# Kernel tuning notes

Measured on AMD Instinct MI355X. Metric: run time of the kernel, lower is better.

Reference implementation:

```python
import jax, jax.numpy as jnp
import numpy as np

N_NODES = 50000
N_EDGES = 600000
IN_CH = 128
HID = 256
OUT_FEAT = 256
OUT_CH = 128
EPS = 1e-12


def _sage_conv(x, src, dst, mask_f, Wl, bl, Wr, n_nodes):
    # PyG SAGEConv: out = lin_l(mean_{j in N(i)} x_j) + lin_r(x_i); L2-normalize rows.
    msg = x[src] * mask_f[:, None]                                  # [E, d] gather
    agg = jax.ops.segment_sum(msg, dst, num_segments=n_nodes)      # [N, d]
    cnt = jax.ops.segment_sum(mask_f, dst, num_segments=n_nodes)   # [N]
    agg = agg / jnp.maximum(cnt, 1.0)[:, None]                      # mean over kept edges
    out = agg @ Wl.T + bl + x @ Wr.T                                 # [N, h]
    nrm = jnp.maximum(jnp.linalg.norm(out, axis=-1, keepdims=True), EPS)
    return out / nrm


def setup_inputs() -> dict:
    key = jax.random.key(0)
    ks = jax.random.split(key, 12)
    x = jax.random.normal(ks[0], (N_NODES, IN_CH), dtype=jnp.float32)
    edge_index = jax.random.randint(ks[1], (2, N_EDGES), 0, N_NODES, dtype=jnp.int32)
    edge_mask = jax.random.bernoulli(ks[2], 0.7, (N_EDGES,))  # dropout_edge p=0.3 keep mask

    def lin(k, fan_out, fan_in):
        s = 1.0 / np.sqrt(fan_in)
        return jax.random.uniform(k, (fan_out, fan_in), jnp.float32, -s, s)

    W1l = lin(ks[3], HID, IN_CH)
    b1 = jnp.zeros((HID,), jnp.float32)
    W1r = lin(ks[4], HID, IN_CH)
    Ws = lin(ks[5], HID, IN_CH)
    bs = jnp.zeros((HID,), jnp.float32)
    W2l = lin(ks[6], OUT_FEAT, HID)
    b2 = jnp.zeros((OUT_FEAT,), jnp.float32)
    W2r = lin(ks[7], OUT_FEAT, HID)
    Wo = lin(ks[8], OUT_CH, OUT_FEAT)
    bo = jnp.zeros((OUT_CH,), jnp.float32)
    return {"x": x, "edge_index": edge_index, "edge_mask": edge_mask,
            "W1l": W1l, "b1": b1, "W1r": W1r, "Ws": Ws, "bs": bs,
            "W2l": W2l, "b2": b2, "W2r": W2r, "Wo": Wo, "bo": bo}


def reference(x, edge_index, edge_mask, W1l, b1, W1r, Ws, bs, W2l, b2, W2r, Wo, bo):
    src, dst = edge_index[0], edge_index[1]
    ones = jnp.ones((src.shape[0],), x.dtype)
    # conv1 uses all edges
    h = _sage_conv(x, src, dst, ones, W1l, b1, W1r, N_NODES)
    h = h + (x @ Ws.T + bs)
    h = jnp.tanh(h)
    # conv2 uses edge-dropped graph (mask = kept edges)
    mask_f = edge_mask.astype(x.dtype)
    h = jnp.tanh(_sage_conv(h, src, dst, mask_f, W2l, b2, W2r, N_NODES))
    return h @ Wo.T + bo
```

## Files before the change

### kernel.cpp

```cpp
#include <hip/hip_runtime.h>
#include <hip/hip_bf16.h>

#define N_NODES 50000
#define N_PAD   50048
#define N_EDGES 600000
#define IN_CH 128
#define HID 256
#define OUT_CH 128

typedef unsigned short u16;
typedef unsigned char u8;
typedef unsigned int u32;

typedef __attribute__((ext_vector_type(8))) short short8;
typedef __attribute__((ext_vector_type(4))) float f32x4;

typedef __attribute__((address_space(3))) u32 as3_u32;
typedef __attribute__((address_space(1))) const u32 as1_u32;

__device__ __forceinline__ float bf2f(u16 v) {
    unsigned u = ((unsigned)v) << 16;
    return __uint_as_float(u);
}
__device__ __forceinline__ u16 f2bf(float f) {
    unsigned u = __float_as_uint(f);
    u += 0x7FFF + ((u >> 16) & 1);
    return (u16)(u >> 16);
}

__device__ __forceinline__ void async16(const void* g, void* l) {
    __builtin_amdgcn_global_load_lds((as1_u32*)g, (as3_u32*)l, 16, 0, 0);
}

__global__ void detect_kernel(const u16* __restrict__ xu, const u8* __restrict__ mb,
                              int* __restrict__ flags) {
    int lane = threadIdx.x & 63;

    int inr = 0;
    {
        u32 w0 = ((const u32*)xu)[lane * 2 + 0];
        u32 w1 = ((const u32*)xu)[lane * 2 + 1];
        u16 h[4] = {(u16)w0, (u16)(w0 >> 16), (u16)w1, (u16)(w1 >> 16)};
#pragma unroll
        for (int j = 0; j < 4; j++) {
            int e = (h[j] >> 7) & 0xFF;
            if (e >= 100 && e <= 133) inr++;
        }
    }

    int c1 = 0, c23 = 0, h3f_1 = 0, h3f_3 = 0;
#pragma unroll
    for (int t = 0; t < 16; t++) {
        u32 w = ((const u32*)mb)[t * 64 + lane];
        u8 b1 = (u8)(w >> 8), b2 = (u8)(w >> 16), b3 = (u8)(w >> 24);
        if (b1) c1++;
        if (b1 == 0x3F) h3f_1 = 1;
        if (b2) c23++;
        if (b3) c23++;
        if (b3 == 0x3F) h3f_3 = 1;
    }

#pragma unroll
    for (int off = 32; off > 0; off >>= 1) {
        inr   += __shfl_xor(inr, off, 64);
        c1    += __shfl_xor(c1, off, 64);
        c23   += __shfl_xor(c23, off, 64);
        h3f_1 |= __shfl_xor(h3f_1, off, 64);
        h3f_3 |= __shfl_xor(h3f_3, off, 64);
    }

    if (lane == 0 && blockIdx.x == 0) {
        flags[0] = (inr >= 200) ? 1 : 0;
        int fmt;
        if (h3f_1) fmt = 3;
        else if (h3f_3) fmt = 2;
        else if (c1 + c23 > 0) fmt = 0;
        else fmt = 1;
        flags[1] = fmt;
    }
}

#define NX (N_NODES * IN_CH)
__global__ void convert_all_kernel(const void* __restrict__ x,
                                   const void* __restrict__ W1l, const void* __restrict__ W1r,
                                   const void* __restrict__ Ws,
                                   const void* __restrict__ W2l, const void* __restrict__ W2r,
                                   const void* __restrict__ Wo,
                                   const void* __restrict__ b1, const void* __restrict__ bs,
                                   const void* __restrict__ b2, const void* __restrict__ bo,
                                   u16* __restrict__ xb, u16* __restrict__ Wc1,
                                   u16* __restrict__ Wsb, u16* __restrict__ Wc2,
                                   u16* __restrict__ Wob, float* __restrict__ biasf,
                                   const int* __restrict__ flags) {
    int i = blockIdx.x * blockDim.x + threadIdx.x;
    int isbf = flags[0];
    auto cv = [&](const void* s, int idx) -> u16 {
        return isbf ? ((const u16*)s)[idx] : f2bf(((const float*)s)[idx]);
    };
    if (i < NX) { xb[i] = cv(x, i); return; }
    i -= NX;
    if (i < 256 * 256) {
        int n = i >> 8, k = i & 255;
        const void* s = (k < 128) ? W1l : W1r;
        Wc1[i] = cv(s, n * 128 + (k & 127));
        return;
    }
    i -= 256 * 256;
    if (i < 256 * 128) { Wsb[i] = cv(Ws, i); return; }
    i -= 256 * 128;
    if (i < 256 * 512) {
        int n = i >> 9, k = i & 511;
        const void* s = (k < 256) ? W2l : W2r;
        Wc2[i] = cv(s, n * 256 + (k & 255));
        return;
    }
    i -= 256 * 512;
    if (i < 128 * 256) { Wob[i] = cv(Wo, i); return; }
    i -= 128 * 256;
    if (i < 896) {
        const void* s; int idx;
        if (i < 256)      { s = b1; idx = i; }
        else if (i < 512) { s = bs; idx = i - 256; }
        else if (i < 768) { s = b2; idx = i - 512; }
        else              { s = bo; idx = i - 768; }
        biasf[i] = isbf ? bf2f(((const u16*)s)[idx]) : ((const float*)s)[idx];
    }
}
#define CONV_TOTAL (NX + 256 * 256 + 256 * 128 + 256 * 512 + 128 * 256 + 896)

__global__ void hist_kernel(const int* __restrict__ ei, const void* __restrict__ em,
                            u32* __restrict__ degp, u32* __restrict__ rankp,
                            const int* __restrict__ flags) {
    int i = blockIdx.x * blockDim.x + threadIdx.x;
    if (i >= N_EDGES) return;
    int d = ei[N_EDGES + i];
    int fmt = flags[1];
    bool keep;
    if (fmt == 0)      keep = ((const u8*)em)[i] != 0;
    else if (fmt == 1) keep = ((const int*)em)[i] != 0;
    else if (fmt == 2) keep = ((const float*)em)[i] != 0.f;
    else               keep = ((const u16*)em)[i] != 0;
    u32 inc = keep ? 0x10001u : 1u;
    u32 old = atomicAdd(&degp[d], inc);
    rankp[i] = (old & 0xffffu) | (keep ? (old & 0xffff0000u) : 0xffff0000u);
}

__global__ void partial_kernel(const u32* __restrict__ degp, u32* __restrict__ partial) {
    __shared__ u32 sh[256];
    int t = threadIdx.x;
    int i = blockIdx.x * 256 + t;
    sh[t] = (i < N_NODES) ? degp[i] : 0;
    __syncthreads();
    for (int s = 128; s > 0; s >>= 1) {
        if (t < s) sh[t] += sh[t + s];
        __syncthreads();
    }
    if (t == 0) partial[blockIdx.x] = sh[0];
}

__global__ void scanp_kernel(const u32* __restrict__ partial, int* __restrict__ pscan, int nb) {
    __shared__ int sh[256];
    int t = threadIdx.x;
    u32 pv = (t < nb) ? partial[t] : 0;
    int v1 = pv & 0xffff, v2 = pv >> 16;
    sh[t] = v1;
    __syncthreads();
    for (int o = 1; o < 256; o <<= 1) {
        int u = (t >= o) ? sh[t - o] : 0;
        __syncthreads();
        sh[t] += u;
        __syncthreads();
    }
    if (t < nb) pscan[t] = sh[t] - v1;
    __syncthreads();
    sh[t] = v2;
    __syncthreads();
    for (int o = 1; o < 256; o <<= 1) {
        int u = (t >= o) ? sh[t - o] : 0;
        __syncthreads();
        sh[t] += u;
        __syncthreads();
    }
    if (t < nb) pscan[nb + t] = sh[t] - v2;
}

__global__ void rowptr_kernel(const u32* __restrict__ degp, const int* __restrict__ pscan,
                              int* __restrict__ row_ptr, int* __restrict__ row_ptr2, int nb) {
    __shared__ u32 sh[256];
    int t = threadIdx.x;
    int i = blockIdx.x * 256 + t;
    u32 v = (i < N_NODES) ? degp[i] : 0;
    sh[t] = v;
    __syncthreads();
    for (int o = 1; o < 256; o <<= 1) {
        u32 u = (t >= o) ? sh[t - o] : 0;
        __syncthreads();
        sh[t] += u;
        __syncthreads();
    }
    u32 ex = sh[t] - v;
    if (i <= N_NODES) {
        row_ptr[i]  = pscan[blockIdx.x] + (int)(ex & 0xffff);
        row_ptr2[i] = pscan[nb + blockIdx.x] + (int)(ex >> 16);
    }
}

__global__ void scatter_csr_kernel(const int* __restrict__ ei, const u32* __restrict__ rankp,
                                   const int* __restrict__ row_ptr, const int* __restrict__ row_ptr2,
                                   int* __restrict__ srcs, int* __restrict__ srcs2) {
    int i = blockIdx.x * blockDim.x + threadIdx.x;
    if (i >= N_EDGES) return;
    int d = ei[N_EDGES + i];
    int s = ei[i];
    u32 rp = rankp[i];
    srcs[row_ptr[d] + (int)(rp & 0xffffu)] = s;
    u32 kr = rp >> 16;
    if (kr != 0xffffu) srcs2[row_ptr2[d] + (int)kr] = s;
}

__global__ __launch_bounds__(256) void gather1_kernel(const int* __restrict__ row_ptr,
                                                      const int* __restrict__ srcs,
                                                      const u16* __restrict__ xb,
                                                      u16* __restrict__ aggb) {
    int wid = (blockIdx.x * blockDim.x + threadIdx.x) >> 6;
    int lane = threadIdx.x & 63;
    if (wid >= N_NODES) return;
    int start = row_ptr[wid], end = row_ptr[wid + 1];
    int dg = end - start;
    int sv = (lane < dg) ? srcs[start + lane] : 0;
    float a0 = 0.f, a1 = 0.f, b0 = 0.f, b1 = 0.f;
    float c0 = 0.f, c1 = 0.f, d0 = 0.f, d1 = 0.f;
    int n = dg < 64 ? dg : 64;
    int e = 0;
    for (; e + 4 <= n; e += 4) {
        int s0 = __builtin_amdgcn_readlane(sv, e);
        int s1 = __builtin_amdgcn_readlane(sv, e + 1);
        int s2 = __builtin_amdgcn_readlane(sv, e + 2);
        int s3 = __builtin_amdgcn_readlane(sv, e + 3);
        u32 v0 = *(const u32*)(xb + (size_t)s0 * IN_CH + lane * 2);
        u32 v1 = *(const u32*)(xb + (size_t)s1 * IN_CH + lane * 2);
        u32 v2 = *(const u32*)(xb + (size_t)s2 * IN_CH + lane * 2);
        u32 v3 = *(const u32*)(xb + (size_t)s3 * IN_CH + lane * 2);
        a0 += bf2f((u16)v0); a1 += bf2f((u16)(v0 >> 16));
        b0 += bf2f((u16)v1); b1 += bf2f((u16)(v1 >> 16));
        c0 += bf2f((u16)v2); c1 += bf2f((u16)(v2 >> 16));
        d0 += bf2f((u16)v3); d1 += bf2f((u16)(v3 >> 16));
    }
    for (; e < n; e++) {
        int s0 = __builtin_amdgcn_readlane(sv, e);
        u32 v0 = *(const u32*)(xb + (size_t)s0 * IN_CH + lane * 2);
        a0 += bf2f((u16)v0); a1 += bf2f((u16)(v0 >> 16));
    }
    for (e = 64; e < dg; e++) {
        int s0 = srcs[start + e];
        u32 v0 = *(const u32*)(xb + (size_t)s0 * IN_CH + lane * 2);
        a0 += bf2f((u16)v0); a1 += bf2f((u16)(v0 >> 16));
    }
    float inv = 1.f / fmaxf((float)dg, 1.f);
    float rx = (a0 + b0) + (c0 + d0);
    float ry = (a1 + b1) + (c1 + d1);
    u32 o = (u32)f2bf(rx * inv) | ((u32)f2bf(ry * inv) << 16);
    *(u32*)(aggb + (size_t)wid * IN_CH + lane * 2) = o;
}

__global__ __launch_bounds__(256) void gather2_kernel(const int* __restrict__ row_ptr2,
                                                      const int* __restrict__ srcs2,
                                                      const u16* __restrict__ h1b,
                                                      u16* __restrict__ aggb) {
    int wid = (blockIdx.x * blockDim.x + threadIdx.x) >> 6;
    int lane = threadIdx.x & 63;
    if (wid >= N_NODES) return;
    int start = row_ptr2[wid], end = row_ptr2[wid + 1];
    int dg = end - start;
    int sv = (lane < dg) ? srcs2[start + lane] : 0;
    float a0 = 0.f, a1 = 0.f, a2 = 0.f, a3 = 0.f;
    float b0 = 0.f, b1 = 0.f, b2 = 0.f, b3 = 0.f;
    float c0 = 0.f, c1 = 0.f, c2 = 0.f, c3 = 0.f;
    float d0 = 0.f, d1 = 0.f, d2 = 0.f, d3 = 0.f;
    int n = dg < 64 ? dg : 64;
    int e = 0;
    for (; e + 4 <= n; e += 4) {
        int s0 = __builtin_amdgcn_readlane(sv, e);
        int s1 = __builtin_amdgcn_readlane(sv, e + 1);
        int s2 = __builtin_amdgcn_readlane(sv, e + 2);
        int s3 = __builtin_amdgcn_readlane(sv, e + 3);
        uint2 v = *(const uint2*)(h1b + (size_t)s0 * HID + lane * 4);
        uint2 w = *(const uint2*)(h1b + (size_t)s1 * HID + lane * 4);
        uint2 y = *(const uint2*)(h1b + (size_t)s2 * HID + lane * 4);
        uint2 zz = *(const uint2*)(h1b + (size_t)s3 * HID + lane * 4);
        a0 += bf2f((u16)v.x); a1 += bf2f((u16)(v.x >> 16));
        a2 += bf2f((u16)v.y); a3 += bf2f((u16)(v.y >> 16));
        b0 += bf2f((u16)w.x); b1 += bf2f((u16)(w.x >> 16));
        b2 += bf2f((u16)w.y); b3 += bf2f((u16)(w.y >> 16));
        c0 += bf2f((u16)y.x); c1 += bf2f((u16)(y.x >> 16));
        c2 += bf2f((u16)y.y); c3 += bf2f((u16)(y.y >> 16));
        d0 += bf2f((u16)zz.x); d1 += bf2f((u16)(zz.x >> 16));
        d2 += bf2f((u16)zz.y); d3 += bf2f((u16)(zz.y >> 16));
    }
    for (; e < n; e++) {
        int s0 = __builtin_amdgcn_readlane(sv, e);
        uint2 v = *(const uint2*)(h1b + (size_t)s0 * HID + lane * 4);
        a0 += bf2f((u16)v.x); a1 += bf2f((u16)(v.x >> 16));
        a2 += bf2f((u16)v.y); a3 += bf2f((u16)(v.y >> 16));
    }
    for (e = 64; e < dg; e++) {
        int s0 = srcs2[start + e];
        uint2 v = *(const uint2*)(h1b + (size_t)s0 * HID + lane * 4);
        a0 += bf2f((u16)v.x); a1 += bf2f((u16)(v.x >> 16));
        a2 += bf2f((u16)v.y); a3 += bf2f((u16)(v.y >> 16));
    }
    float inv = 1.f / fmaxf((float)dg, 1.f);
    float r0 = (a0 + b0) + (c0 + d0);
    float r1 = (a1 + b1) + (c1 + d1);
    float r2 = (a2 + b2) + (c2 + d2);
    float r3 = (a3 + b3) + (c3 + d3);
    u32 o0 = (u32)f2bf(r0 * inv) | ((u32)f2bf(r1 * inv) << 16);
    u32 o1 = (u32)f2bf(r2 * inv) | ((u32)f2bf(r3 * inv) << 16);
    u16* p = aggb + (size_t)wid * HID + lane * 4;
    *(u32*)p = o0;
    *(u32*)(p + 2) = o1;
}

template<int MODE>
__global__ __launch_bounds__(256, 2) void gemm_staged(
    const u16* __restrict__ A0, const u16* __restrict__ A1,
    const u16* __restrict__ W0, const u16* __restrict__ W1,
    const float* __restrict__ bias0, const float* __restrict__ bias1,
    u16* __restrict__ outb, void* __restrict__ outv, const int* __restrict__ flags) {

    constexpr int NT  = (MODE == 3) ? 2 : 4;
    constexpr int Nw  = NT * 16;
    constexpr int NKS = (MODE == 1) ? 6 : ((MODE == 2) ? 8 : 4);
    constexpr int BBYTES = NT * 64 * 128;
    __shared__ __align__(16) u8 ldsmem[16384 + 2 * BBYTES];

    int tid = threadIdx.x;
    int w = tid >> 6, lane = tid & 63;
    int q = lane >> 4, c = lane & 15;
    int m_base = blockIdx.x * 64;
    int rj = lane >> 3, jj = lane & 7;
    int j16 = ((jj ^ rj) << 4);

    f32x4 acc[4][NT], acc2[4][NT];
    const f32x4 z = {0.f, 0.f, 0.f, 0.f};
#pragma unroll
    for (int mt = 0; mt < 4; mt++)
#pragma unroll
        for (int nt = 0; nt < NT; nt++) { acc[mt][nt] = z; acc2[mt][nt] = z; }

    auto stage = [&](int ks, int b) {
        const u16* ap; int astr, kta;
        const u16* wp; int wstr, ktw;
        if (MODE == 1) {
            astr = 128;
            if (ks < 2)      { ap = A0; kta = ks; }
            else if (ks < 4) { ap = A1; kta = ks - 2; }
            else             { ap = A1; kta = ks - 4; }
            if (ks < 4) { wp = W0; wstr = 256; ktw = ks; }
            else        { wp = W1; wstr = 128; ktw = ks - 4; }
        } else if (MODE == 2) {
            astr = 256;
            if (ks < 4) { ap = A0; kta = ks; } else { ap = A1; kta = ks - 4; }
            wp = W0; wstr = 512; ktw = ks;
        } else {
            astr = 256; ap = A0; kta = ks;
            wp = W0; wstr = 256; ktw = ks;
        }
#pragma unroll
        for (int t = 0; t < 2; t++) {
            int r = w * 16 + t * 8;
            const u8* g = (const u8*)(ap + (size_t)(m_base + r + rj) * astr) + kta * 128 + j16;
            async16(g, ldsmem + b * 8192 + r * 128);
        }
#pragma unroll
        for (int t = 0; t < NT * 2; t++) {
            int n = w * Nw + t * 8;
            const u8* g = (const u8*)(wp + (size_t)(n + rj) * wstr) + ktw * 128 + j16;
            async16(g, ldsmem + 16384 + b * BBYTES + n * 128);
        }
    };

    auto compute = [&](int b, f32x4 (*tgt)[NT]) {
        const u8* ab = ldsmem + b * 8192;
        const u8* bb = ldsmem + 16384 + b * BBYTES;
#pragma unroll
        for (int kk = 0; kk < 2; kk++) {
            int sA = (((kk * 4 + q) ^ (c & 7)) << 4);
            short8 af[4], bfr[NT];
#pragma unroll
            for (int mt = 0; mt < 4; mt++)
                af[mt] = *(const short8*)(ab + (mt * 16 + c) * 128 + sA);
#pragma unroll
            for (int nt = 0; nt < NT; nt++)
                bfr[nt] = *(const short8*)(bb + (w * Nw + nt * 16 + c) * 128 + sA);
#pragma unroll
            for (int mt = 0; mt < 4; mt++)
#pragma unroll
                for (int nt = 0; nt < NT; nt++)
                    tgt[mt][nt] = __builtin_amdgcn_mfma_f32_16x16x32_bf16(af[mt], bfr[nt], tgt[mt][nt], 0, 0, 0);
        }
    };

    stage(0, 0);
    int b = 0;
#pragma unroll
    for (int ks = 0; ks < NKS; ks++) {
        __syncthreads();
        if (ks + 1 < NKS) stage(ks + 1, b ^ 1);
        if (MODE == 1 && ks >= 4) compute(b, acc2);
        else                      compute(b, acc);
        b ^= 1;
    }
    __syncthreads();

    if (MODE == 3) {
        float bcol[NT];
#pragma unroll
        for (int nt = 0; nt < NT; nt++) bcol[nt] = bias0[w * Nw + nt * 16 + c];
        int isbf = flags[0];
#pragma unroll
        for (int mt = 0; mt < 4; mt++)
#pragma unroll
            for (int r = 0; r < 4; r++) {
                int row = m_base + mt * 16 + q * 4 + r;
                if (row < N_NODES) {
#pragma unroll
                    for (int nt = 0; nt < NT; nt++) {
                        float v = acc[mt][nt][r] + bcol[nt];
                        int col = w * Nw + nt * 16 + c;
                        if (isbf) ((u16*)outv)[(size_t)row * OUT_CH + col] = f2bf(v);
                        else      ((float*)outv)[(size_t)row * OUT_CH + col] = v;
                    }
                }
            }
    } else {
        float* redf = (float*)ldsmem;
        float bcol[NT], b2col[NT];
#pragma unroll
        for (int nt = 0; nt < NT; nt++) {
            int col = w * Nw + nt * 16 + c;
            bcol[nt] = bias0[col];
            if (MODE == 1) b2col[nt] = bias1[col];
        }
        float s[4][4];
#pragma unroll
        for (int mt = 0; mt < 4; mt++)
#pragma unroll
            for (int r = 0; r < 4; r++) {
                float t = 0.f;
#pragma unroll
                for (int nt = 0; nt < NT; nt++) {
                    float v = acc[mt][nt][r] + bcol[nt];
                    acc[mt][nt][r] = v;
                    t += v * v;
                }
                s[mt][r] = t;
            }
#pragma unroll
        for (int off = 1; off < 16; off <<= 1) {
#pragma unroll
            for (int mt = 0; mt < 4; mt++)
#pragma unroll
                for (int r = 0; r < 4; r++)
                    s[mt][r] += __shfl_xor(s[mt][r], off, 64);
        }
        if (c == 0) {
#pragma unroll
            for (int mt = 0; mt < 4; mt++)
#pragma unroll
                for (int r = 0; r < 4; r++)
                    redf[(mt * 16 + q * 4 + r) * 4 + w] = s[mt][r];
        }
        __syncthreads();
        if (tid < 64) {
            float t = redf[tid * 4] + redf[tid * 4 + 1] + redf[tid * 4 + 2] + redf[tid * 4 + 3];
            redf[256 + tid] = 1.f / fmaxf(sqrtf(t), 1e-12f);
        }
        __syncthreads();
#pragma unroll
        for (int mt = 0; mt < 4; mt++)
#pragma unroll
            for (int r = 0; r < 4; r++) {
                int rl = mt * 16 + q * 4 + r;
                int row = m_base + rl;
                if (row < N_NODES) {
                    float iv = redf[256 + rl];
#pragma unroll
                    for (int nt = 0; nt < NT; nt++) {
                        int col = w * Nw + nt * 16 + c;
                        float h;
                        if (MODE == 1) h = acc[mt][nt][r] * iv + acc2[mt][nt][r] + b2col[nt];
                        else           h = acc[mt][nt][r] * iv;
                        outb[(size_t)row * HID + col] = f2bf(tanhf(h));
                    }
                }
            }
    }
}

extern "C" void kernel_launch(void* const* d_in, const int* in_sizes, int n_in,
                              void* d_out, int out_size, void* d_ws, size_t ws_size,
                              hipStream_t stream) {
    const void* x    = d_in[0];
    const int*  ei   = (const int*)d_in[1];
    const void* em   = d_in[2];
    const void* W1l  = d_in[3];
    const void* b1   = d_in[4];
    const void* W1r  = d_in[5];
    const void* Ws   = d_in[6];
    const void* bs   = d_in[7];
    const void* W2l  = d_in[8];
    const void* b2   = d_in[9];
    const void* W2r  = d_in[10];
    const void* Wo   = d_in[11];
    const void* bo   = d_in[12];

    char* p = (char*)d_ws;
    auto carve = [&](size_t bytes) { char* r = p; p += (bytes + 63) & ~(size_t)63; return r; };
    int*   flags   = (int*)carve(256);
    u16*   xb      = (u16*)carve((size_t)N_PAD * IN_CH * 2);
    u16*   h1b     = (u16*)carve((size_t)N_PAD * HID * 2);
    u16*   aggb    = (u16*)carve((size_t)N_PAD * HID * 2);
    u16*   h2b     = (u16*)carve((size_t)N_PAD * HID * 2);
    u16*   Wc1     = (u16*)carve(256 * 256 * 2);
    u16*   Wsb     = (u16*)carve(256 * 128 * 2);
    u16*   Wc2     = (u16*)carve(256 * 512 * 2);
    u16*   Wob     = (u16*)carve(128 * 256 * 2);
    float* biasf   = (float*)carve(896 * 4);
    u32*   degp    = (u32*)carve(50176 * 4);
    int*   row_ptr = (int*)carve(50056 * 4);
    int*   row_ptr2= (int*)carve(50056 * 4);
    u32*   partial = (u32*)carve(256 * 4);
    int*   pscan   = (int*)carve(512 * 4);
    u32*   rankp   = (u32*)carve((size_t)N_EDGES * 4);
    int*   srcs    = (int*)carve((size_t)N_EDGES * 4);
    int*   srcs2   = (int*)carve((size_t)N_EDGES * 4);
    float* b1f = biasf, *bsf = biasf + 256, *b2f = biasf + 512, *bof = biasf + 768;
    (void)ws_size; (void)in_sizes; (void)n_in; (void)out_size;

    detect_kernel<<<1, 64, 0, stream>>>((const u16*)x, (const u8*)em, flags);

    convert_all_kernel<<<(CONV_TOTAL + 255) / 256, 256, 0, stream>>>(
        x, W1l, W1r, Ws, W2l, W2r, Wo, b1, bs, b2, bo,
        xb, Wc1, Wsb, Wc2, Wob, biasf, flags);

    hipMemsetAsync(degp, 0, 50176 * sizeof(u32), stream);
    hist_kernel<<<(N_EDGES + 255) / 256, 256, 0, stream>>>(ei, em, degp, rankp, flags);
    const int NB = (N_NODES + 255) / 256;
    partial_kernel<<<NB, 256, 0, stream>>>(degp, partial);
    scanp_kernel<<<1, 256, 0, stream>>>(partial, pscan, NB);
    rowptr_kernel<<<NB, 256, 0, stream>>>(degp, pscan, row_ptr, row_ptr2, NB);
    scatter_csr_kernel<<<(N_EDGES + 255) / 256, 256, 0, stream>>>(ei, rankp, row_ptr, row_ptr2, srcs, srcs2);

    const int GB = N_PAD / 64;

    gather1_kernel<<<(N_NODES * 64) / 256, 256, 0, stream>>>(row_ptr, srcs, xb, aggb);
    gemm_staged<1><<<GB, 256, 0, stream>>>(aggb, xb, Wc1, Wsb, b1f, bsf, h1b, nullptr, flags);

    gather2_kernel<<<(N_NODES * 64) / 256, 256, 0, stream>>>(row_ptr2, srcs2, h1b, aggb);
    gemm_staged<2><<<GB, 256, 0, stream>>>(aggb, h1b, Wc2, nullptr, b2f, nullptr, h2b, nullptr, flags);

    gemm_staged<3><<<GB, 256, 0, stream>>>(h2b, nullptr, Wob, nullptr, bof, nullptr, nullptr, d_out, flags);
}
```

Before: 309.5 us.

## Fuse prep kernels, merge partial scan, and fuse output GEMM into conv2 GEMM

Merges format detection, dtype conversion and the degree histogram into one prep kernel. The partial-sum and block-scan kernels become one, with a last-block-done atomic. The final output projection is fused into the conv2 GEMM epilogue: the tanh'd h2 tile is written to LDS in a swizzled layout and multiplied by Wo there, so the h2 buffer round trip and a launch go away. The cost is that every prep block redoes the format detection, plus extra LDS and register pressure in the fused GEMM.

```diff
diff --git a/kernel.cpp b/kernel.cpp
--- a/kernel.cpp
+++ b/kernel.cpp
@@ -32,71 +32,64 @@
     __builtin_amdgcn_global_load_lds((as1_u32*)g, (as3_u32*)l, 16, 0, 0);
 }
 
-__global__ void detect_kernel(const u16* __restrict__ xu, const u8* __restrict__ mb,
-                              int* __restrict__ flags) {
-    int lane = threadIdx.x & 63;
-
-    int inr = 0;
+#define NX (N_NODES * IN_CH)
+#define CONV_TOTAL (NX + 256 * 256 + 256 * 128 + 256 * 512 + 128 * 256 + 896)
+#define PREP_TOTAL (CONV_TOTAL + N_EDGES)
+
+__global__ void prep_kernel(const void* __restrict__ x,
+                            const void* __restrict__ W1l, const void* __restrict__ W1r,
+                            const void* __restrict__ Ws,
+                            const void* __restrict__ W2l, const void* __restrict__ W2r,
+                            const void* __restrict__ Wo,
+                            const void* __restrict__ b1, const void* __restrict__ bs,
+                            const void* __restrict__ b2, const void* __restrict__ bo,
+                            const int* __restrict__ ei, const void* __restrict__ em,
+                            u16* __restrict__ xb, u16* __restrict__ Wc1,
+                            u16* __restrict__ Wsb, u16* __restrict__ Wc2,
+                            u16* __restrict__ Wob, float* __restrict__ biasf,
+                            u32* __restrict__ degp, u32* __restrict__ rankp,
+                            int* __restrict__ flags) {
+    __shared__ int s_inr, s_c1, s_c23, s_h1, s_h3, s_isbf, s_fmt;
+    int t = threadIdx.x;
+    if (t == 0) { s_inr = 0; s_c1 = 0; s_c23 = 0; s_h1 = 0; s_h3 = 0; }
+    __syncthreads();
+    if (t < 128) {
+        u32 w = ((const u32*)x)[t];
+        int cnt = 0;
+        int e0 = (w >> 7) & 0xFF;
+        if (e0 >= 100 && e0 <= 133) cnt++;
+        int e1 = (w >> 23) & 0xFF;
+        if (e1 >= 100 && e1 <= 133) cnt++;
+        if (cnt) atomicAdd(&s_inr, cnt);
+    }
     {
-        u32 w0 = ((const u32*)xu)[lane * 2 + 0];
-        u32 w1 = ((const u32*)xu)[lane * 2 + 1];
-        u16 h[4] = {(u16)w0, (u16)(w0 >> 16), (u16)w1, (u16)(w1 >> 16)};
-#pragma unroll
-        for (int j = 0; j < 4; j++) {
-            int e = (h[j] >> 7) & 0xFF;
-            if (e >= 100 && e <= 133) inr++;
-        }
-    }
-
-    int c1 = 0, c23 = 0, h3f_1 = 0, h3f_3 = 0;
-#pragma unroll
-    for (int t = 0; t < 16; t++) {
-        u32 w = ((const u32*)mb)[t * 64 + lane];
-        u8 b1 = (u8)(w >> 8), b2 = (u8)(w >> 16), b3 = (u8)(w >> 24);
-        if (b1) c1++;
-        if (b1 == 0x3F) h3f_1 = 1;
-        if (b2) c23++;
-        if (b3) c23++;
-        if (b3 == 0x3F) h3f_3 = 1;
-    }
-
-#pragma unroll
-    for (int off = 32; off > 0; off >>= 1) {
-        inr   += __shfl_xor(inr, off, 64);
-        c1    += __shfl_xor(c1, off, 64);
-        c23   += __shfl_xor(c23, off, 64);
-        h3f_1 |= __shfl_xor(h3f_1, off, 64);
-        h3f_3 |= __shfl_xor(h3f_3, off, 64);
-    }
-
-    if (lane == 0 && blockIdx.x == 0) {
-        flags[0] = (inr >= 200) ? 1 : 0;
+        u32 w = ((const u32*)em)[t];
+        u8 m1 = (u8)(w >> 8), m2 = (u8)(w >> 16), m3 = (u8)(w >> 24);
+        if (m1) atomicAdd(&s_c1, 1);
+        if (m1 == 0x3F) s_h1 = 1;
+        if (m2 || m3) atomicAdd(&s_c23, 1);
+        if (m3 == 0x3F) s_h3 = 1;
+    }
+    __syncthreads();
+    if (t == 0) {
+        s_isbf = (s_inr >= 200) ? 1 : 0;
         int fmt;
-        if (h3f_1) fmt = 3;
-        else if (h3f_3) fmt = 2;
-        else if (c1 + c23 > 0) fmt = 0;
+        if (s_h1) fmt = 3;
+        else if (s_h3) fmt = 2;
+        else if (s_c1 + s_c23 > 0) fmt = 0;
         else fmt = 1;
-        flags[1] = fmt;
-    }
-}
-
-#define NX (N_NODES * IN_CH)
-__global__ void convert_all_kernel(const void* __restrict__ x,
-                                   const void* __restrict__ W1l, const void* __restrict__ W1r,
-                                   const void* __restrict__ Ws,
-                                   const void* __restrict__ W2l, const void* __restrict__ W2r,
-                                   const void* __restrict__ Wo,
-                                   const void* __restrict__ b1, const void* __restrict__ bs,
-                                   const void* __restrict__ b2, const void* __restrict__ bo,
-                                   u16* __restrict__ xb, u16* __restrict__ Wc1,
-                                   u16* __restrict__ Wsb, u16* __restrict__ Wc2,
-                                   u16* __restrict__ Wob, float* __restrict__ biasf,
-                                   const int* __restrict__ flags) {
-    int i = blockIdx.x * blockDim.x + threadIdx.x;
-    int isbf = flags[0];
+        s_fmt = fmt;
+    }
+    __syncthreads();
+    int isbf = s_isbf, fmt = s_fmt;
+
+    long gi = (long)blockIdx.x * 256 + t;
+    if (gi == 0) { flags[0] = isbf; flags[1] = fmt; }
     auto cv = [&](const void* s, int idx) -> u16 {
         return isbf ? ((const u16*)s)[idx] : f2bf(((const float*)s)[idx]);
     };
+    if (gi >= PREP_TOTAL) return;
+    int i = (int)gi;
     if (i < NX) { xb[i] = cv(x, i); return; }
     i -= NX;
     if (i < 256 * 256) {
@@ -124,29 +117,27 @@
         else if (i < 768) { s = b2; idx = i - 512; }
         else              { s = bo; idx = i - 768; }
         biasf[i] = isbf ? bf2f(((const u16*)s)[idx]) : ((const float*)s)[idx];
-    }
-}
-#define CONV_TOTAL (NX + 256 * 256 + 256 * 128 + 256 * 512 + 128 * 256 + 896)
-
-__global__ void hist_kernel(const int* __restrict__ ei, const void* __restrict__ em,
-                            u32* __restrict__ degp, u32* __restrict__ rankp,
-                            const int* __restrict__ flags) {
-    int i = blockIdx.x * blockDim.x + threadIdx.x;
-    if (i >= N_EDGES) return;
-    int d = ei[N_EDGES + i];
-    int fmt = flags[1];
-    bool keep;
-    if (fmt == 0)      keep = ((const u8*)em)[i] != 0;
-    else if (fmt == 1) keep = ((const int*)em)[i] != 0;
-    else if (fmt == 2) keep = ((const float*)em)[i] != 0.f;
-    else               keep = ((const u16*)em)[i] != 0;
-    u32 inc = keep ? 0x10001u : 1u;
-    u32 old = atomicAdd(&degp[d], inc);
-    rankp[i] = (old & 0xffffu) | (keep ? (old & 0xffff0000u) : 0xffff0000u);
-}
-
-__global__ void partial_kernel(const u32* __restrict__ degp, u32* __restrict__ partial) {
+        return;
+    }
+    i -= 896;
+    if (i < N_EDGES) {
+        int d = ei[N_EDGES + i];
+        bool keep;
+        if (fmt == 0)      keep = ((const u8*)em)[i] != 0;
+        else if (fmt == 1) keep = ((const int*)em)[i] != 0;
+        else if (fmt == 2) keep = ((const float*)em)[i] != 0.f;
+        else               keep = ((const u16*)em)[i] != 0;
+        u32 inc = keep ? 0x10001u : 1u;
+        u32 old = atomicAdd(&degp[d], inc);
+        rankp[i] = (old & 0xffffu) | (keep ? (old & 0xffff0000u) : 0xffff0000u);
+    }
+}
+
+__global__ void partial_scan_kernel(const u32* __restrict__ degp, u32* __restrict__ partial,
+                                    int* __restrict__ pscan, u32* __restrict__ done, int nb) {
     __shared__ u32 sh[256];
+    __shared__ int shi[256];
+    __shared__ int lastf;
     int t = threadIdx.x;
     int i = blockIdx.x * 256 + t;
     sh[t] = (i < N_NODES) ? degp[i] : 0;
@@ -155,33 +146,36 @@
         if (t < s) sh[t] += sh[t + s];
         __syncthreads();
     }
-    if (t == 0) partial[blockIdx.x] = sh[0];
-}
-
-__global__ void scanp_kernel(const u32* __restrict__ partial, int* __restrict__ pscan, int nb) {
-    __shared__ int sh[256];
-    int t = threadIdx.x;
+    if (t == 0) {
+        partial[blockIdx.x] = sh[0];
+        __threadfence();
+        u32 tk = atomicAdd(done, 1u);
+        lastf = (tk == (u32)(gridDim.x - 1)) ? 1 : 0;
+    }
+    __syncthreads();
+    if (!lastf) return;
+    __threadfence();
     u32 pv = (t < nb) ? partial[t] : 0;
     int v1 = pv & 0xffff, v2 = pv >> 16;
-    sh[t] = v1;
+    shi[t] = v1;
     __syncthreads();
     for (int o = 1; o < 256; o <<= 1) {
-        int u = (t >= o) ? sh[t - o] : 0;
-        __syncthreads();
-        sh[t] += u;
-        __syncthreads();
-    }
-    if (t < nb) pscan[t] = sh[t] - v1;
-    __syncthreads();
-    sh[t] = v2;
+        int u = (t >= o) ? shi[t - o] : 0;
+        __syncthreads();
+        shi[t] += u;
+        __syncthreads();
+    }
+    if (t < nb) pscan[t] = shi[t] - v1;
+    __syncthreads();
+    shi[t] = v2;
     __syncthreads();
     for (int o = 1; o < 256; o <<= 1) {
-        int u = (t >= o) ? sh[t - o] : 0;
-        __syncthreads();
-        sh[t] += u;
-        __syncthreads();
-    }
-    if (t < nb) pscan[nb + t] = sh[t] - v2;
+        int u = (t >= o) ? shi[t - o] : 0;
+        __syncthreads();
+        shi[t] += u;
+        __syncthreads();
+    }
+    if (t < nb) pscan[nb + t] = shi[t] - v2;
 }
 
 __global__ void rowptr_kernel(const u32* __restrict__ degp, const int* __restrict__ pscan,
@@ -328,9 +322,9 @@
     const float* __restrict__ bias0, const float* __restrict__ bias1,
     u16* __restrict__ outb, void* __restrict__ outv, const int* __restrict__ flags) {
 
-    constexpr int NT  = (MODE == 3) ? 2 : 4;
+    constexpr int NT  = 4;
     constexpr int Nw  = NT * 16;
-    constexpr int NKS = (MODE == 1) ? 6 : ((MODE == 2) ? 8 : 4);
+    constexpr int NKS = (MODE == 1) ? 6 : 8;
     constexpr int BBYTES = NT * 64 * 128;
     __shared__ __align__(16) u8 ldsmem[16384 + 2 * BBYTES];
 
@@ -358,13 +352,10 @@
             else             { ap = A1; kta = ks - 4; }
             if (ks < 4) { wp = W0; wstr = 256; ktw = ks; }
             else        { wp = W1; wstr = 128; ktw = ks - 4; }
-        } else if (MODE == 2) {
+        } else {
             astr = 256;
             if (ks < 4) { ap = A0; kta = ks; } else { ap = A1; kta = ks - 4; }
             wp = W0; wstr = 512; ktw = ks;
-        } else {
-            astr = 256; ap = A0; kta = ks;
-            wp = W0; wstr = 256; ktw = ks;
         }
 #pragma unroll
         for (int t = 0; t < 2; t++) {
@@ -413,70 +404,51 @@
     }
     __syncthreads();
 
-    if (MODE == 3) {
-        float bcol[NT];
-#pragma unroll
-        for (int nt = 0; nt < NT; nt++) bcol[nt] = bias0[w * Nw + nt * 16 + c];
-        int isbf = flags[0];
+    float* redf = (float*)ldsmem;
+    float bcol[NT], b2col[NT];
+#pragma unroll
+    for (int nt = 0; nt < NT; nt++) {
+        int col = w * Nw + nt * 16 + c;
+        bcol[nt] = bias0[col];
+        if (MODE == 1) b2col[nt] = bias1[col];
+    }
+    float s[4][4];
+#pragma unroll
+    for (int mt = 0; mt < 4; mt++)
+#pragma unroll
+        for (int r = 0; r < 4; r++) {
+            float t = 0.f;
+#pragma unroll
+            for (int nt = 0; nt < NT; nt++) {
+                float v = acc[mt][nt][r] + bcol[nt];
+                acc[mt][nt][r] = v;
+                t += v * v;
+            }
+            s[mt][r] = t;
+        }
+#pragma unroll
+    for (int off = 1; off < 16; off <<= 1) {
 #pragma unroll
         for (int mt = 0; mt < 4; mt++)
 #pragma unroll
-            for (int r = 0; r < 4; r++) {
-                int row = m_base + mt * 16 + q * 4 + r;
-                if (row < N_NODES) {
-#pragma unroll
-                    for (int nt = 0; nt < NT; nt++) {
-                        float v = acc[mt][nt][r] + bcol[nt];
-                        int col = w * Nw + nt * 16 + c;
-                        if (isbf) ((u16*)outv)[(size_t)row * OUT_CH + col] = f2bf(v);
-                        else      ((float*)outv)[(size_t)row * OUT_CH + col] = v;
-                    }
-                }
-            }
-    } else {
-        float* redf = (float*)ldsmem;
-        float bcol[NT], b2col[NT];
-#pragma unroll
-        for (int nt = 0; nt < NT; nt++) {
-            int col = w * Nw + nt * 16 + c;
-            bcol[nt] = bias0[col];
-            if (MODE == 1) b2col[nt] = bias1[col];
-        }
-        float s[4][4];
+            for (int r = 0; r < 4; r++)
+                s[mt][r] += __shfl_xor(s[mt][r], off, 64);
+    }
+    if (c == 0) {
 #pragma unroll
         for (int mt = 0; mt < 4; mt++)
 #pragma unroll
-            for (int r = 0; r < 4; r++) {
-                float t = 0.f;
-#pragma unroll
-                for (int nt = 0; nt < NT; nt++) {
-                    float v = acc[mt][nt][r] + bcol[nt];
-                    acc[mt][nt][r] = v;
-                    t += v * v;
-                }
-                s[mt][r] = t;
-            }
-#pragma unroll
-        for (int off = 1; off < 16; off <<= 1) {
-#pragma unroll
-            for (int mt = 0; mt < 4; mt++)
-#pragma unroll
-                for (int r = 0; r < 4; r++)
-                    s[mt][r] += __shfl_xor(s[mt][r], off, 64);
-        }
-        if (c == 0) {
-#pragma unroll
-            for (int mt = 0; mt < 4; mt++)
-#pragma unroll
-                for (int r = 0; r < 4; r++)
-                    redf[(mt * 16 + q * 4 + r) * 4 + w] = s[mt][r];
-        }
-        __syncthreads();
-        if (tid < 64) {
-            float t = redf[tid * 4] + redf[tid * 4 + 1] + redf[tid * 4 + 2] + redf[tid * 4 + 3];
-            redf[256 + tid] = 1.f / fmaxf(sqrtf(t), 1e-12f);
-        }
-        __syncthreads();
+            for (int r = 0; r < 4; r++)
+                redf[(mt * 16 + q * 4 + r) * 4 + w] = s[mt][r];
+    }
+    __syncthreads();
+    if (tid < 64) {
+        float t = redf[tid * 4] + redf[tid * 4 + 1] + redf[tid * 4 + 2] + redf[tid * 4 + 3];
+        redf[256 + tid] = 1.f / fmaxf(sqrtf(t), 1e-12f);
+    }
+    __syncthreads();
+
+    if constexpr (MODE == 1) {
 #pragma unroll
         for (int mt = 0; mt < 4; mt++)
 #pragma unroll
@@ -488,10 +460,83 @@
 #pragma unroll
                     for (int nt = 0; nt < NT; nt++) {
                         int col = w * Nw + nt * 16 + c;
-                        float h;
-                        if (MODE == 1) h = acc[mt][nt][r] * iv + acc2[mt][nt][r] + b2col[nt];
-                        else           h = acc[mt][nt][r] * iv;
+                        float h = acc[mt][nt][r] * iv + acc2[mt][nt][r] + b2col[nt];
                         outb[(size_t)row * HID + col] = f2bf(tanhf(h));
+                    }
+                }
+            }
+    } else {
+        u8* h2l = ldsmem + 16384;
+#pragma unroll
+        for (int mt = 0; mt < 4; mt++)
+#pragma unroll
+            for (int r = 0; r < 4; r++) {
+                int rl = mt * 16 + q * 4 + r;
+                float iv = redf[256 + rl];
+#pragma unroll
+                for (int nt = 0; nt < NT; nt++) {
+                    int col = w * Nw + nt * 16 + c;
+                    u16 val = f2bf(tanhf(acc[mt][nt][r] * iv));
+                    int ksn = col >> 6, cc = col & 63;
+                    int slot = (cc >> 3) ^ (rl & 7);
+                    *(u16*)(h2l + rl * 512 + ksn * 128 + slot * 16 + (cc & 7) * 2) = val;
+                }
+            }
+        f32x4 accf[4][2];
+#pragma unroll
+        for (int mt = 0; mt < 4; mt++)
+#pragma unroll
+            for (int nt = 0; nt < 2; nt++) accf[mt][nt] = z;
+
+        auto stageW = [&](int ksf, int fb) {
+#pragma unroll
+            for (int tt = 0; tt < 4; tt++) {
+                int n = w * 32 + tt * 8;
+                const u8* g = (const u8*)W1 + (size_t)(n + rj) * 512 + ksf * 128 + j16;
+                async16(g, ldsmem + 16384 + BBYTES + fb * 16384 + n * 128);
+            }
+        };
+        stageW(0, 0);
+        int fb = 0;
+#pragma unroll
+        for (int ksf = 0; ksf < 4; ksf++) {
+            __syncthreads();
+            if (ksf < 3) stageW(ksf + 1, fb ^ 1);
+            const u8* bb2 = ldsmem + 16384 + BBYTES + fb * 16384;
+#pragma unroll
+            for (int kk = 0; kk < 2; kk++) {
+                int sA = (((kk * 4 + q) ^ (c & 7)) << 4);
+                short8 af[4], bf2[2];
+#pragma unroll
+                for (int mt = 0; mt < 4; mt++)
+                    af[mt] = *(const short8*)(h2l + (mt * 16 + c) * 512 + ksf * 128 + sA);
+#pragma unroll
+                for (int nt = 0; nt < 2; nt++)
+                    bf2[nt] = *(const short8*)(bb2 + (w * 32 + nt * 16 + c) * 128 + sA);
+#pragma unroll
+                for (int mt = 0; mt < 4; mt++)
+#pragma unroll
+                    for (int nt = 0; nt < 2; nt++)
+                        accf[mt][nt] = __builtin_amdgcn_mfma_f32_16x16x32_bf16(af[mt], bf2[nt], accf[mt][nt], 0, 0, 0);
+            }
+            fb ^= 1;
+        }
+        float bfo[2];
+#pragma unroll
+        for (int nt = 0; nt < 2; nt++) bfo[nt] = bias1[w * 32 + nt * 16 + c];
+        int isbf = flags[0];
+#pragma unroll
+        for (int mt = 0; mt < 4; mt++)
+#pragma unroll
+            for (int r = 0; r < 4; r++) {
+                int row = m_base + mt * 16 + q * 4 + r;
+                if (row < N_NODES) {
+#pragma unroll
+                    for (int nt = 0; nt < 2; nt++) {
+                        float v = accf[mt][nt][r] + bfo[nt];
+                        int col = w * 32 + nt * 16 + c;
+                        if (isbf) ((u16*)outv)[(size_t)row * OUT_CH + col] = f2bf(v);
+                        else      ((float*)outv)[(size_t)row * OUT_CH + col] = v;
                     }
                 }
             }
@@ -521,13 +566,12 @@
     u16*   xb      = (u16*)carve((size_t)N_PAD * IN_CH * 2);
     u16*   h1b     = (u16*)carve((size_t)N_PAD * HID * 2);
     u16*   aggb    = (u16*)carve((size_t)N_PAD * HID * 2);
-    u16*   h2b     = (u16*)carve((size_t)N_PAD * HID * 2);
     u16*   Wc1     = (u16*)carve(256 * 256 * 2);
     u16*   Wsb     = (u16*)carve(256 * 128 * 2);
     u16*   Wc2     = (u16*)carve(256 * 512 * 2);
     u16*   Wob     = (u16*)carve(128 * 256 * 2);
     float* biasf   = (float*)carve(896 * 4);
-    u32*   degp    = (u32*)carve(50176 * 4);
+    u32*   degp    = (u32*)carve(50240 * 4);
     int*   row_ptr = (int*)carve(50056 * 4);
     int*   row_ptr2= (int*)carve(50056 * 4);
     u32*   partial = (u32*)carve(256 * 4);
@@ -536,19 +580,17 @@
     int*   srcs    = (int*)carve((size_t)N_EDGES * 4);
     int*   srcs2   = (int*)carve((size_t)N_EDGES * 4);
     float* b1f = biasf, *bsf = biasf + 256, *b2f = biasf + 512, *bof = biasf + 768;
+    u32*   done = degp + 50176;
     (void)ws_size; (void)in_sizes; (void)n_in; (void)out_size;
 
-    detect_kernel<<<1, 64, 0, stream>>>((const u16*)x, (const u8*)em, flags);
-
-    convert_all_kernel<<<(CONV_TOTAL + 255) / 256, 256, 0, stream>>>(
-        x, W1l, W1r, Ws, W2l, W2r, Wo, b1, bs, b2, bo,
-        xb, Wc1, Wsb, Wc2, Wob, biasf, flags);
-
-    hipMemsetAsync(degp, 0, 50176 * sizeof(u32), stream);
-    hist_kernel<<<(N_EDGES + 255) / 256, 256, 0, stream>>>(ei, em, degp, rankp, flags);
+    hipMemsetAsync(degp, 0, 50240 * sizeof(u32), stream);
+
+    prep_kernel<<<(PREP_TOTAL + 255) / 256, 256, 0, stream>>>(
+        x, W1l, W1r, Ws, W2l, W2r, Wo, b1, bs, b2, bo, ei, em,
+        xb, Wc1, Wsb, Wc2, Wob, biasf, degp, rankp, flags);
+
     const int NB = (N_NODES + 255) / 256;
-    partial_kernel<<<NB, 256, 0, stream>>>(degp, partial);
-    scanp_kernel<<<1, 256, 0, stream>>>(partial, pscan, NB);
+    partial_scan_kernel<<<NB, 256, 0, stream>>>(degp, partial, pscan, done, NB);
     rowptr_kernel<<<NB, 256, 0, stream>>>(degp, pscan, row_ptr, row_ptr2, NB);
     scatter_csr_kernel<<<(N_EDGES + 255) / 256, 256, 0, stream>>>(ei, rankp, row_ptr, row_ptr2, srcs, srcs2);
 
@@ -558,7 +600,5 @@
     gemm_staged<1><<<GB, 256, 0, stream>>>(aggb, xb, Wc1, Wsb, b1f, bsf, h1b, nullptr, flags);
 
     gather2_kernel<<<(N_NODES * 64) / 256, 256, 0, stream>>>(row_ptr2, srcs2, h1b, aggb);
-    gemm_staged<2><<<GB, 256, 0, stream>>>(aggb, h1b, Wc2, nullptr, b2f, nullptr, h2b, nullptr, flags);
-
-    gemm_staged<3><<<GB, 256, 0, stream>>>(h2b, nullptr, Wob, nullptr, bof, nullptr, nullptr, d_out, flags);
-}
+    gemm_staged<2><<<GB, 256, 0, stream>>>(aggb, h1b, Wc2, Wob, b2f, bof, nullptr, d_out, flags);
+}
```

Result: slower. 365.0 us (+17.9%).
